# Performance work log

Measured on AMD Instinct MI355X. Metric: run time of the kernel, lower is better.

Reference implementation:

```python
import jax, jax.numpy as jnp
import numpy as np


def setup_inputs() -> dict:
    key = jax.random.key(0)
    k1, k2, k3, k4, k5 = jax.random.split(key, 5)
    B, S, D, U = 64, 2048, 512, 512
    he = lambda k, shape: jax.random.normal(k, shape, dtype=jnp.float32) * jnp.sqrt(2.0 / shape[0])
    return {
        "query": jax.random.normal(k1, (B, D), dtype=jnp.float32),
        "values": jax.random.normal(k2, (B, S, D), dtype=jnp.float32),
        "W1": he(k3, (D, U)),
        "W2": he(k4, (D, U)),
        "V1": he(k5, (U, 1)),
    }


def reference(query, values, W1, W2, V1):
    # query: (B, D), values: (B, S, D)
    Q = query @ W1                       # (B, U)
    V = jnp.einsum("bsd,du->bsu", values, W2)  # (B, S, U)
    add = jnp.tanh(Q[:, None, :] + V)    # (B, S, U)
    score = jnp.einsum("bsu,uo->bso", add, V1)  # (B, S, 1)
    attn = jax.nn.softmax(score, axis=1)         # (B, S, 1)
    context = jnp.sum(attn * values, axis=1)     # (B, D)
    return context
```

## Files before the change

kernel.cpp:

```cpp
#include <hip/hip_runtime.h>
#include <hip/hip_bf16.h>


typedef __attribute__((ext_vector_type(8))) short bf16x8;
typedef __attribute__((ext_vector_type(4))) float f32x4;

#if __has_builtin(__builtin_amdgcn_exp2f)
__device__ __forceinline__ float fast_exp2(float x) { return __builtin_amdgcn_exp2f(x); }
#else
__device__ __forceinline__ float fast_exp2(float x) { return exp2f(x); }
#endif
#if __has_builtin(__builtin_amdgcn_rcpf)
__device__ __forceinline__ float fast_rcp(float x) { return __builtin_amdgcn_rcpf(x); }
#else
__device__ __forceinline__ float fast_rcp(float x) { return 1.0f / x; }
#endif

__device__ __forceinline__ unsigned short f2bf(float f) {
  unsigned int u = __float_as_uint(f);
  u += 0x7fffu + ((u >> 16) & 1u);
  return (unsigned short)(u >> 16);
}

__device__ __forceinline__ unsigned int cvt_pk_bf16(float a, float b) {
  const __hip_bfloat16 lo = __float2bfloat16(a);
  const __hip_bfloat16 hi = __float2bfloat16(b);
  const unsigned short ul = *reinterpret_cast<const unsigned short*>(&lo);
  const unsigned short uh = *reinterpret_cast<const unsigned short*>(&hi);
  return (unsigned int)ul | ((unsigned int)uh << 16);
}

__global__ __launch_bounds__(256) void prep_k(
    const float* __restrict__ query, const float* __restrict__ W1,
    const float* __restrict__ W2, float* __restrict__ Q,
    unsigned short* __restrict__ Wtf) {
  __shared__ float qrow[512];
  const int t = threadIdx.x;
  if (blockIdx.x < 128) {
    const int b = blockIdx.x >> 1, half = blockIdx.x & 1;
    qrow[t] = query[b * 512 + t];
    qrow[t + 256] = query[b * 512 + t + 256];
    __syncthreads();
    const int u = half * 256 + t;
    float acc = 0.f;
#pragma unroll 8
    for (int k = 0; k < 512; ++k) acc += qrow[k] * W1[(size_t)k * 512 + u];
    Q[b * 512 + u] = acc;
  } else {
    const int gid = (blockIdx.x - 128) * 256 + t;
    const int lane = gid & 63;
    const int g = gid >> 6;
    const int ks = g & 15, ntile = g >> 4;
    const int l15 = lane & 15, quad = lane >> 4;
    const int n = ntile * 16 + l15;
    const int k0 = ks * 32 + quad * 8;
    unsigned int p[4];
#pragma unroll
    for (int jj = 0; jj < 4; ++jj) {
      const float a = W2[(size_t)(k0 + 2 * jj) * 512 + n];
      const float b = W2[(size_t)(k0 + 2 * jj + 1) * 512 + n];
      p[jj] = (unsigned int)f2bf(a) | ((unsigned int)f2bf(b) << 16);
    }
    *(uint4*)&Wtf[(size_t)gid * 8] = make_uint4(p[0], p[1], p[2], p[3]);
  }
}

__global__ __launch_bounds__(512, 4) void scorectx_k(
    const float* __restrict__ values, const unsigned short* __restrict__ Wtf,
    const float* __restrict__ Q, const float* __restrict__ V1,
    float* __restrict__ Pstat, float* __restrict__ Pctx) {
  __shared__ __align__(16) unsigned short Ab[64 * 512];
  __shared__ float sAcc[64];
  __shared__ float wLDS[64];

  const int t = threadIdx.x;
  const int lane = t & 63;
  const int w = t >> 6;
  const int quad = lane >> 4;
  const int l15 = lane & 15;
  const int blk = blockIdx.x;
  const int m0 = blk * 64;
  const int b = m0 >> 11;

  if (t < 64) sAcc[t] = 0.0f;

  const float* Ag = values + (size_t)m0 * 512;
#pragma unroll
  for (int i = 0; i < 8; ++i) {
    const int c = i * 512 + t;
    const int m = c >> 6;
    const int kc = c & 63;
    const float4* src = (const float4*)(Ag + (size_t)m * 512 + kc * 8);
    const float4 x = src[0], y = src[1];
    const unsigned int p0 = cvt_pk_bf16(x.x, x.y);
    const unsigned int p1 = cvt_pk_bf16(x.z, x.w);
    const unsigned int p2 = cvt_pk_bf16(y.x, y.y);
    const unsigned int p3 = cvt_pk_bf16(y.z, y.w);
    *(uint4*)&Ab[m * 512 + ((kc ^ (m & 7)) * 8)] = make_uint4(p0, p1, p2, p3);
  }
  __syncthreads();

  f32x4 acc[4][4];
#pragma unroll
  for (int mt = 0; mt < 4; ++mt)
#pragma unroll
    for (int nt = 0; nt < 4; ++nt) acc[mt][nt] = (f32x4){0.f, 0.f, 0.f, 0.f};

  const unsigned short* Bg = Wtf + (size_t)lane * 8;
  const int sw = l15 & 7;

#pragma unroll
  for (int ks = 0; ks < 16; ++ks) {
    bf16x8 bfr[4], af[4];
#pragma unroll
    for (int nt = 0; nt < 4; ++nt)
      bfr[nt] = *(const bf16x8*)(Bg + (size_t)((w * 4 + nt) * 16 + ks) * 512);
#pragma unroll
    for (int mt = 0; mt < 4; ++mt) {
      const int m = mt * 16 + l15;
      af[mt] = *(const bf16x8*)&Ab[m * 512 + (((ks * 4 + quad) ^ sw) * 8)];
    }
#pragma unroll
    for (int mt = 0; mt < 4; ++mt)
#pragma unroll
      for (int nt = 0; nt < 4; ++nt)
        acc[mt][nt] = __builtin_amdgcn_mfma_f32_16x16x32_bf16(af[mt], bfr[nt],
                                                              acc[mt][nt], 0, 0, 0);
  }

  float part[4][4];
#pragma unroll
  for (int mt = 0; mt < 4; ++mt)
#pragma unroll
    for (int r = 0; r < 4; ++r) part[mt][r] = 0.f;

#pragma unroll
  for (int nt = 0; nt < 4; ++nt) {
    const int n = w * 64 + nt * 16 + l15;
    const float qv = Q[b * 512 + n];
    const float v1 = V1[n];
#pragma unroll
    for (int mt = 0; mt < 4; ++mt)
#pragma unroll
      for (int r = 0; r < 4; ++r) {
        const float x = acc[mt][nt][r] + qv;
        const float e = fast_exp2(x * 2.8853900817779268f);
        const float th = 1.0f - 2.0f * fast_rcp(e + 1.0f);
        part[mt][r] += th * v1;
      }
  }
#pragma unroll
  for (int mt = 0; mt < 4; ++mt)
#pragma unroll
    for (int r = 0; r < 4; ++r) {
      float v = part[mt][r];
      v += __shfl_xor(v, 1);
      v += __shfl_xor(v, 2);
      v += __shfl_xor(v, 4);
      v += __shfl_xor(v, 8);
      if (l15 == 0) atomicAdd(&sAcc[mt * 16 + quad * 4 + r], v);
    }
  __syncthreads();

  const float L2E = 1.4426950408889634f;
  if (t < 64) {
    const float v = sAcc[t];
    float m = v;
#pragma unroll
    for (int o = 1; o < 64; o <<= 1) m = fmaxf(m, __shfl_xor(m, o));
    const float wv = fast_exp2((v - m) * L2E);
    float dsum = wv;
#pragma unroll
    for (int o = 1; o < 64; o <<= 1) dsum += __shfl_xor(dsum, o);
    wLDS[t] = wv;
    if (t == 0) {
      Pstat[2 * blk] = m;
      Pstat[2 * blk + 1] = dsum;
    }
  }
  __syncthreads();

  const float* vrow = values + (size_t)m0 * 512 + t;
  float cacc = 0.f;
#pragma unroll 8
  for (int r = 0; r < 64; ++r) cacc += wLDS[r] * vrow[(size_t)r * 512];
  Pctx[(size_t)blk * 512 + t] = cacc;
}

__global__ __launch_bounds__(512) void comb_k(const float* __restrict__ Pstat,
                                              const float* __restrict__ Pctx,
                                              float* __restrict__ out) {
  __shared__ float aL[32];
  __shared__ float Dsh;
  const int b = blockIdx.x, t = threadIdx.x;
  const float L2E = 1.4426950408889634f;
  if (t < 32) {
    const float2 st = ((const float2*)Pstat)[b * 32 + t];
    float m = st.x;
#pragma unroll
    for (int o = 1; o < 32; o <<= 1) m = fmaxf(m, __shfl_xor(m, o));
    const float a = fast_exp2((st.x - m) * L2E);
    float D = a * st.y;
#pragma unroll
    for (int o = 1; o < 32; o <<= 1) D += __shfl_xor(D, o);
    aL[t] = a;
    if (t == 0) Dsh = D;
  }
  __syncthreads();
  const float* pc = Pctx + (size_t)b * 32 * 512 + t;
  float acc = 0.f;
#pragma unroll
  for (int i = 0; i < 32; ++i) acc += aL[i] * pc[(size_t)i * 512];
  out[b * 512 + t] = acc / Dsh;
}

extern "C" void kernel_launch(void* const* d_in, const int* in_sizes, int n_in,
                              void* d_out, int out_size, void* d_ws, size_t ws_size,
                              hipStream_t stream) {
  const float* query = (const float*)d_in[0];
  const float* values = (const float*)d_in[1];
  const float* W1 = (const float*)d_in[2];
  const float* W2 = (const float*)d_in[3];
  const float* V1 = (const float*)d_in[4];
  float* out = (float*)d_out;

  char* ws = (char*)d_ws;
  float* Qp = (float*)ws;
  unsigned short* Wtp = (unsigned short*)(ws + 131072);
  float* Pstat = (float*)(ws + 131072 + 524288);
  float* Pctx = (float*)(ws + 131072 + 524288 + 16384);

  prep_k<<<256, 256, 0, stream>>>(query, W1, W2, Qp, Wtp);
  scorectx_k<<<2048, 512, 0, stream>>>(values, Wtp, Qp, V1, Pstat, Pctx);
  comb_k<<<64, 512, 0, stream>>>(Pstat, Pctx, out);
}
```

Baseline: 477.0 us.

## Double-buffer values tiles in LDS to overlap global loads with MFMA

```diff
diff --git a/kernel.cpp b/kernel.cpp
--- a/kernel.cpp
+++ b/kernel.cpp
@@ -65,11 +65,11 @@
   }
 }
 
-__global__ __launch_bounds__(512, 4) void scorectx_k(
+__global__ __launch_bounds__(512) void scorectx_k(
     const float* __restrict__ values, const unsigned short* __restrict__ Wtf,
     const float* __restrict__ Q, const float* __restrict__ V1,
     float* __restrict__ Pstat, float* __restrict__ Pctx) {
-  __shared__ __align__(16) unsigned short Ab[64 * 512];
+  __shared__ __align__(16) unsigned short Ab[2][64 * 128];
   __shared__ float sAcc[64];
   __shared__ float wLDS[64];
 
@@ -84,19 +84,26 @@
 
   if (t < 64) sAcc[t] = 0.0f;
 
-  const float* Ag = values + (size_t)m0 * 512;
-#pragma unroll
-  for (int i = 0; i < 8; ++i) {
-    const int c = i * 512 + t;
-    const int m = c >> 6;
-    const int kc = c & 63;
-    const float4* src = (const float4*)(Ag + (size_t)m * 512 + kc * 8);
-    const float4 x = src[0], y = src[1];
-    const unsigned int p0 = cvt_pk_bf16(x.x, x.y);
-    const unsigned int p1 = cvt_pk_bf16(x.z, x.w);
-    const unsigned int p2 = cvt_pk_bf16(y.x, y.y);
-    const unsigned int p3 = cvt_pk_bf16(y.z, y.w);
-    *(uint4*)&Ab[m * 512 + ((kc ^ (m & 7)) * 8)] = make_uint4(p0, p1, p2, p3);
+  const int sm = t >> 3;
+  const int sp = t & 7;
+  const int sk = sm & 7;
+  const float* src = values + (size_t)(m0 + sm) * 512 + sp * 16;
+  const int wo0 = sm * 128 + (((2 * sp) ^ sk) * 8);
+  const int wo1 = sm * 128 + (((2 * sp + 1) ^ sk) * 8);
+
+  {
+    const f32x4* s4 = (const f32x4*)src;
+    const f32x4 r0 = s4[0], r1 = s4[1], r2 = s4[2], r3 = s4[3];
+    const unsigned int p0 = cvt_pk_bf16(r0[0], r0[1]);
+    const unsigned int p1 = cvt_pk_bf16(r0[2], r0[3]);
+    const unsigned int p2 = cvt_pk_bf16(r1[0], r1[1]);
+    const unsigned int p3 = cvt_pk_bf16(r1[2], r1[3]);
+    const unsigned int p4 = cvt_pk_bf16(r2[0], r2[1]);
+    const unsigned int p5 = cvt_pk_bf16(r2[2], r2[3]);
+    const unsigned int p6 = cvt_pk_bf16(r3[0], r3[1]);
+    const unsigned int p7 = cvt_pk_bf16(r3[2], r3[3]);
+    *(uint4*)&Ab[0][wo0] = make_uint4(p0, p1, p2, p3);
+    *(uint4*)&Ab[0][wo1] = make_uint4(p4, p5, p6, p7);
   }
   __syncthreads();
 
@@ -110,22 +117,49 @@
   const int sw = l15 & 7;
 
 #pragma unroll
-  for (int ks = 0; ks < 16; ++ks) {
-    bf16x8 bfr[4], af[4];
-#pragma unroll
-    for (int nt = 0; nt < 4; ++nt)
-      bfr[nt] = *(const bf16x8*)(Bg + (size_t)((w * 4 + nt) * 16 + ks) * 512);
-#pragma unroll
-    for (int mt = 0; mt < 4; ++mt) {
-      const int m = mt * 16 + l15;
-      af[mt] = *(const bf16x8*)&Ab[m * 512 + (((ks * 4 + quad) ^ sw) * 8)];
-    }
-#pragma unroll
-    for (int mt = 0; mt < 4; ++mt)
+  for (int c = 0; c < 4; ++c) {
+    f32x4 r0, r1, r2, r3;
+    if (c < 3) {
+      const f32x4* s4 = (const f32x4*)(src + (c + 1) * 128);
+      r0 = s4[0];
+      r1 = s4[1];
+      r2 = s4[2];
+      r3 = s4[3];
+      asm volatile("" : "+v"(r0), "+v"(r1), "+v"(r2), "+v"(r3));
+    }
+
+    const unsigned short* Ac = &Ab[c & 1][0];
+#pragma unroll
+    for (int kl = 0; kl < 4; ++kl) {
+      const int ks = c * 4 + kl;
+      bf16x8 bfr[4], af[4];
 #pragma unroll
       for (int nt = 0; nt < 4; ++nt)
-        acc[mt][nt] = __builtin_amdgcn_mfma_f32_16x16x32_bf16(af[mt], bfr[nt],
-                                                              acc[mt][nt], 0, 0, 0);
+        bfr[nt] = *(const bf16x8*)(Bg + (size_t)((w * 4 + nt) * 16 + ks) * 512);
+#pragma unroll
+      for (int mt = 0; mt < 4; ++mt)
+        af[mt] = *(const bf16x8*)&Ac[(mt * 16 + l15) * 128 + (((kl * 4 + quad) ^ sw) * 8)];
+#pragma unroll
+      for (int mt = 0; mt < 4; ++mt)
+#pragma unroll
+        for (int nt = 0; nt < 4; ++nt)
+          acc[mt][nt] = __builtin_amdgcn_mfma_f32_16x16x32_bf16(af[mt], bfr[nt],
+                                                                acc[mt][nt], 0, 0, 0);
+    }
+
+    if (c < 3) {
+      const unsigned int p0 = cvt_pk_bf16(r0[0], r0[1]);
+      const unsigned int p1 = cvt_pk_bf16(r0[2], r0[3]);
+      const unsigned int p2 = cvt_pk_bf16(r1[0], r1[1]);
+      const unsigned int p3 = cvt_pk_bf16(r1[2], r1[3]);
+      const unsigned int p4 = cvt_pk_bf16(r2[0], r2[1]);
+      const unsigned int p5 = cvt_pk_bf16(r2[2], r2[3]);
+      const unsigned int p6 = cvt_pk_bf16(r3[0], r3[1]);
+      const unsigned int p7 = cvt_pk_bf16(r3[2], r3[3]);
+      *(uint4*)&Ab[(c + 1) & 1][wo0] = make_uint4(p0, p1, p2, p3);
+      *(uint4*)&Ab[(c + 1) & 1][wo1] = make_uint4(p4, p5, p6, p7);
+    }
+    __syncthreads();
   }
 
   float part[4][4];
```

After: 492.7 us. +3.3%, slower.

## Double-buffer K-chunks of values in LDS with 1024-thread blocks and prefetching

Applied to the files above, without the earlier changes.

```diff
diff --git a/kernel.cpp b/kernel.cpp
--- a/kernel.cpp
+++ b/kernel.cpp
@@ -65,13 +65,14 @@
   }
 }
 
-__global__ __launch_bounds__(512, 4) void scorectx_k(
+__global__ __launch_bounds__(1024, 4) void scorectx_k(
     const float* __restrict__ values, const unsigned short* __restrict__ Wtf,
     const float* __restrict__ Q, const float* __restrict__ V1,
     float* __restrict__ Pstat, float* __restrict__ Pctx) {
-  __shared__ __align__(16) unsigned short Ab[64 * 512];
+  __shared__ __align__(16) unsigned short Ab[2][64 * 128];
   __shared__ float sAcc[64];
   __shared__ float wLDS[64];
+  __shared__ float pLDS[1024];
 
   const int t = threadIdx.x;
   const int lane = t & 63;
@@ -84,59 +85,92 @@
 
   if (t < 64) sAcc[t] = 0.0f;
 
-  const float* Ag = values + (size_t)m0 * 512;
-#pragma unroll
-  for (int i = 0; i < 8; ++i) {
-    const int c = i * 512 + t;
-    const int m = c >> 6;
-    const int kc = c & 63;
-    const float4* src = (const float4*)(Ag + (size_t)m * 512 + kc * 8);
-    const float4 x = src[0], y = src[1];
-    const unsigned int p0 = cvt_pk_bf16(x.x, x.y);
-    const unsigned int p1 = cvt_pk_bf16(x.z, x.w);
-    const unsigned int p2 = cvt_pk_bf16(y.x, y.y);
-    const unsigned int p3 = cvt_pk_bf16(y.z, y.w);
-    *(uint4*)&Ab[m * 512 + ((kc ^ (m & 7)) * 8)] = make_uint4(p0, p1, p2, p3);
-  }
-  __syncthreads();
-
-  f32x4 acc[4][4];
+  const int sm = t >> 4;
+  const int sp = t & 15;
+  const int sk = sm & 7;
+  const float* src = values + (size_t)(m0 + sm) * 512 + sp * 8;
+  const int wo = sm * 128 + ((sp ^ sk) * 8);
+
+  {
+    const f32x4 x = *(const f32x4*)src;
+    const f32x4 y = *(const f32x4*)(src + 4);
+    *(uint4*)&Ab[0][wo] = make_uint4(cvt_pk_bf16(x[0], x[1]), cvt_pk_bf16(x[2], x[3]),
+                                     cvt_pk_bf16(y[0], y[1]), cvt_pk_bf16(y[2], y[3]));
+  }
+  __syncthreads();
+
+  f32x4 acc[4][2];
+#pragma unroll
+  for (int mt = 0; mt < 4; ++mt) {
+    acc[mt][0] = (f32x4){0.f, 0.f, 0.f, 0.f};
+    acc[mt][1] = (f32x4){0.f, 0.f, 0.f, 0.f};
+  }
+
+  const int sw = l15 & 7;
+  const unsigned short* B0 = Wtf + (size_t)(w * 2) * 16 * 512 + (size_t)lane * 8;
+  const unsigned short* B1 = B0 + (size_t)16 * 512;
+
+  bf16x8 bc0 = *(const bf16x8*)B0;
+  bf16x8 bc1 = *(const bf16x8*)B1;
+
+#pragma unroll
+  for (int c = 0; c < 4; ++c) {
+    f32x4 sx, sy;
+    if (c < 3) {
+      sx = *(const f32x4*)(src + (c + 1) * 128);
+      sy = *(const f32x4*)(src + (c + 1) * 128 + 4);
+    }
+
+    const unsigned short* Ac = &Ab[c & 1][0];
+    bf16x8 af[4], an[4];
+#pragma unroll
+    for (int mt = 0; mt < 4; ++mt)
+      af[mt] = *(const bf16x8*)&Ac[(mt * 16 + l15) * 128 + ((quad ^ sw) * 8)];
+
+#pragma unroll
+    for (int kl = 0; kl < 4; ++kl) {
+      const int ks = c * 4 + kl;
+      bf16x8 bn0, bn1;
+      if (ks < 15) {
+        bn0 = *(const bf16x8*)(B0 + (size_t)(ks + 1) * 512);
+        bn1 = *(const bf16x8*)(B1 + (size_t)(ks + 1) * 512);
+      }
+      if (kl < 3) {
+#pragma unroll
+        for (int mt = 0; mt < 4; ++mt)
+          an[mt] = *(const bf16x8*)&Ac[(mt * 16 + l15) * 128 +
+                                       ((((kl + 1) * 4 + quad) ^ sw) * 8)];
+      }
+#pragma unroll
+      for (int mt = 0; mt < 4; ++mt) {
+        acc[mt][0] = __builtin_amdgcn_mfma_f32_16x16x32_bf16(af[mt], bc0, acc[mt][0], 0, 0, 0);
+        acc[mt][1] = __builtin_amdgcn_mfma_f32_16x16x32_bf16(af[mt], bc1, acc[mt][1], 0, 0, 0);
+      }
+      bc0 = bn0;
+      bc1 = bn1;
+      if (kl < 3) {
+#pragma unroll
+        for (int mt = 0; mt < 4; ++mt) af[mt] = an[mt];
+      }
+    }
+
+    if (c < 3) {
+      *(uint4*)&Ab[(c + 1) & 1][wo] =
+          make_uint4(cvt_pk_bf16(sx[0], sx[1]), cvt_pk_bf16(sx[2], sx[3]),
+                     cvt_pk_bf16(sy[0], sy[1]), cvt_pk_bf16(sy[2], sy[3]));
+    }
+    __syncthreads();
+  }
+
+  float part[4][4];
 #pragma unroll
   for (int mt = 0; mt < 4; ++mt)
 #pragma unroll
-    for (int nt = 0; nt < 4; ++nt) acc[mt][nt] = (f32x4){0.f, 0.f, 0.f, 0.f};
-
-  const unsigned short* Bg = Wtf + (size_t)lane * 8;
-  const int sw = l15 & 7;
-
-#pragma unroll
-  for (int ks = 0; ks < 16; ++ks) {
-    bf16x8 bfr[4], af[4];
-#pragma unroll
-    for (int nt = 0; nt < 4; ++nt)
-      bfr[nt] = *(const bf16x8*)(Bg + (size_t)((w * 4 + nt) * 16 + ks) * 512);
-#pragma unroll
-    for (int mt = 0; mt < 4; ++mt) {
-      const int m = mt * 16 + l15;
-      af[mt] = *(const bf16x8*)&Ab[m * 512 + (((ks * 4 + quad) ^ sw) * 8)];
-    }
-#pragma unroll
-    for (int mt = 0; mt < 4; ++mt)
-#pragma unroll
-      for (int nt = 0; nt < 4; ++nt)
-        acc[mt][nt] = __builtin_amdgcn_mfma_f32_16x16x32_bf16(af[mt], bfr[nt],
-                                                              acc[mt][nt], 0, 0, 0);
-  }
-
-  float part[4][4];
-#pragma unroll
-  for (int mt = 0; mt < 4; ++mt)
-#pragma unroll
     for (int r = 0; r < 4; ++r) part[mt][r] = 0.f;
 
 #pragma unroll
-  for (int nt = 0; nt < 4; ++nt) {
-    const int n = w * 64 + nt * 16 + l15;
+  for (int nt = 0; nt < 2; ++nt) {
+    const int n = (w * 2 + nt) * 16 + l15;
     const float qv = Q[b * 512 + n];
     const float v1 = V1[n];
 #pragma unroll
@@ -180,11 +214,17 @@
   }
   __syncthreads();
 
-  const float* vrow = values + (size_t)m0 * 512 + t;
-  float cacc = 0.f;
+  {
+    const int rh = t >> 9;
+    const int col = t & 511;
+    const float* vrow = values + (size_t)(m0 + rh * 32) * 512 + col;
+    float cacc = 0.f;
 #pragma unroll 8
-  for (int r = 0; r < 64; ++r) cacc += wLDS[r] * vrow[(size_t)r * 512];
-  Pctx[(size_t)blk * 512 + t] = cacc;
+    for (int r = 0; r < 32; ++r) cacc += wLDS[rh * 32 + r] * vrow[(size_t)r * 512];
+    pLDS[t] = cacc;
+  }
+  __syncthreads();
+  if (t < 512) Pctx[(size_t)blk * 512 + t] = pLDS[t] + pLDS[t + 512];
 }
 
 __global__ __launch_bounds__(512) void comb_k(const float* __restrict__ Pstat,
@@ -231,6 +271,6 @@
   float* Pctx = (float*)(ws + 131072 + 524288 + 16384);
 
   prep_k<<<256, 256, 0, stream>>>(query, W1, W2, Qp, Wtp);
-  scorectx_k<<<2048, 512, 0, stream>>>(values, Wtp, Qp, V1, Pstat, Pctx);
+  scorectx_k<<<2048, 1024, 0, stream>>>(values, Wtp, Qp, V1, Pstat, Pctx);
   comb_k<<<64, 512, 0, stream>>>(Pstat, Pctx, out);
 }
```

Result: no change. 475.7 us (-0.3%).

## Double-buffer fp32 value tiles via async global-to-LDS loads, convert at fragment read

Applied to the files above, without the earlier changes.

```diff
diff --git a/kernel.cpp b/kernel.cpp
--- a/kernel.cpp
+++ b/kernel.cpp
@@ -4,6 +4,9 @@
 
 typedef __attribute__((ext_vector_type(8))) short bf16x8;
 typedef __attribute__((ext_vector_type(4))) float f32x4;
+
+#define GLOBAL_AS __attribute__((address_space(1)))
+#define LDS_AS __attribute__((address_space(3)))
 
 #if __has_builtin(__builtin_amdgcn_exp2f)
 __device__ __forceinline__ float fast_exp2(float x) { return __builtin_amdgcn_exp2f(x); }
@@ -69,7 +72,7 @@
     const float* __restrict__ values, const unsigned short* __restrict__ Wtf,
     const float* __restrict__ Q, const float* __restrict__ V1,
     float* __restrict__ Pstat, float* __restrict__ Pctx) {
-  __shared__ __align__(16) unsigned short Ab[64 * 512];
+  __shared__ __align__(16) float Ab[2][64 * 128];
   __shared__ float sAcc[64];
   __shared__ float wLDS[64];
 
@@ -84,20 +87,24 @@
 
   if (t < 64) sAcc[t] = 0.0f;
 
-  const float* Ag = values + (size_t)m0 * 512;
-#pragma unroll
-  for (int i = 0; i < 8; ++i) {
-    const int c = i * 512 + t;
-    const int m = c >> 6;
-    const int kc = c & 63;
-    const float4* src = (const float4*)(Ag + (size_t)m * 512 + kc * 8);
-    const float4 x = src[0], y = src[1];
-    const unsigned int p0 = cvt_pk_bf16(x.x, x.y);
-    const unsigned int p1 = cvt_pk_bf16(x.z, x.w);
-    const unsigned int p2 = cvt_pk_bf16(y.x, y.y);
-    const unsigned int p3 = cvt_pk_bf16(y.z, y.w);
-    *(uint4*)&Ab[m * 512 + ((kc ^ (m & 7)) * 8)] = make_uint4(p0, p1, p2, p3);
-  }
+  const int srow = (lane >> 5);
+  const int sslot = lane & 31;
+  const float* vbase = values + (size_t)m0 * 512;
+
+#define STAGE_CHUNK(buf, c)                                                          \
+  {                                                                                  \
+    _Pragma("unroll") for (int j = 0; j < 4; ++j) {                                  \
+      const int r = (w * 4 + j) * 2 + srow;                                          \
+      const int kc = sslot ^ (r & 7);                                                \
+      const float* gsrc = vbase + (size_t)r * 512 + (c) * 128 + kc * 4;              \
+      LDS_AS unsigned int* ldst =                                                    \
+          (LDS_AS unsigned int*)&Ab[buf][(w * 4 + j) * 256];                         \
+      __builtin_amdgcn_global_load_lds((const GLOBAL_AS unsigned int*)gsrc, ldst,    \
+                                       16, 0, 0);                                    \
+    }                                                                                \
+  }
+
+  STAGE_CHUNK(0, 0)
   __syncthreads();
 
   f32x4 acc[4][4];
@@ -110,22 +117,42 @@
   const int sw = l15 & 7;
 
 #pragma unroll
-  for (int ks = 0; ks < 16; ++ks) {
-    bf16x8 bfr[4], af[4];
-#pragma unroll
-    for (int nt = 0; nt < 4; ++nt)
-      bfr[nt] = *(const bf16x8*)(Bg + (size_t)((w * 4 + nt) * 16 + ks) * 512);
-#pragma unroll
-    for (int mt = 0; mt < 4; ++mt) {
-      const int m = mt * 16 + l15;
-      af[mt] = *(const bf16x8*)&Ab[m * 512 + (((ks * 4 + quad) ^ sw) * 8)];
-    }
-#pragma unroll
-    for (int mt = 0; mt < 4; ++mt)
+  for (int c = 0; c < 4; ++c) {
+    if (c < 3) STAGE_CHUNK((c + 1) & 1, c + 1)
+
+    const float* Ac = &Ab[c & 1][0];
+#pragma unroll
+    for (int kl = 0; kl < 4; ++kl) {
+      const int ks = c * 4 + kl;
+      bf16x8 bfr[4], af[4];
 #pragma unroll
       for (int nt = 0; nt < 4; ++nt)
-        acc[mt][nt] = __builtin_amdgcn_mfma_f32_16x16x32_bf16(af[mt], bfr[nt],
-                                                              acc[mt][nt], 0, 0, 0);
+        bfr[nt] = *(const bf16x8*)(Bg + (size_t)((w * 4 + nt) * 16 + ks) * 512);
+#pragma unroll
+      for (int mt = 0; mt < 4; ++mt) {
+        const int m = mt * 16 + l15;
+        const int kc0 = kl * 8 + quad * 2;
+        const int s0 = kc0 ^ sw;
+        const f32x4 f0 = *(const f32x4*)&Ac[m * 128 + ((s0) << 2)];
+        const f32x4 f1 = *(const f32x4*)&Ac[m * 128 + ((s0 ^ 1) << 2)];
+        union {
+          unsigned int d[4];
+          bf16x8 v;
+        } u;
+        u.d[0] = cvt_pk_bf16(f0[0], f0[1]);
+        u.d[1] = cvt_pk_bf16(f0[2], f0[3]);
+        u.d[2] = cvt_pk_bf16(f1[0], f1[1]);
+        u.d[3] = cvt_pk_bf16(f1[2], f1[3]);
+        af[mt] = u.v;
+      }
+#pragma unroll
+      for (int mt = 0; mt < 4; ++mt)
+#pragma unroll
+        for (int nt = 0; nt < 4; ++nt)
+          acc[mt][nt] = __builtin_amdgcn_mfma_f32_16x16x32_bf16(af[mt], bfr[nt],
+                                                                acc[mt][nt], 0, 0, 0);
+    }
+    __syncthreads();
   }
 
   float part[4][4];
@@ -185,6 +212,7 @@
 #pragma unroll 8
   for (int r = 0; r < 64; ++r) cacc += wLDS[r] * vrow[(size_t)r * 512];
   Pctx[(size_t)blk * 512 + t] = cacc;
+#undef STAGE_CHUNK
 }
 
 __global__ __launch_bounds__(512) void comb_k(const float* __restrict__ Pstat,
```

Result: slower. 516.7 us (+8.3%).
